# Kernel tuning notes

Measured on AMD Instinct MI355X. Metric: run time of the kernel, lower is better.

The kernel has to match this reference:

```python
import jax, jax.numpy as jnp
import numpy as np

Q_SCALE = 64  # 1 << 6, from quantize_8bit default
Q_STEP = 2.0 / Q_SCALE
Q_MIN = -(2 ** 7) / Q_SCALE      # -128/64 = -2.0
Q_MAX = (2 ** 7 - 1) / Q_SCALE   # 127/64


def quantize_8bit(x):
    # round-to-step with straight-through estimator (matches slayer quantize), then clamp
    xq = x + jax.lax.stop_gradient(jnp.round(x / Q_STEP) * Q_STEP - x)
    return jnp.clip(xq, Q_MIN, Q_MAX)


def weight_norm(v, g):
    # per-output-channel weight norm: w = g * v / ||v||  (v: [out, in])
    n = jnp.sqrt(jnp.sum(v * v, axis=1, keepdims=True))
    return g[:, None] * v / n


def sigma_delta_block(x, v, g, clamp6):
    # x: [N, Cin, H, W, T]
    qw = quantize_8bit(weight_norm(v, g))           # [Cout, Cin], 8-bit quantized
    y = jnp.einsum('oi,nihwt->nohwt', qw, x)        # 1x1x1 conv (pointwise)
    s = jnp.cumsum(y, axis=-1)                      # sigma unit: accumulate over time
    mean = jnp.mean(s, axis=(0, 2, 3, 4), keepdims=True)  # mean-only batchnorm
    a = s - mean
    if clamp6:                                      # Clamp6 activation (fc2); Ind = identity (fc1)
        a = jnp.clip(a, -6.0, 6.0)
    # delta unit, threshold=0: d[t] = a[t] - a[t-1], a[-1] = 0
    d = jnp.diff(a, axis=-1, prepend=jnp.zeros_like(a[..., :1]))
    return d


def setup_inputs() -> dict:
    key = jax.random.key(0)
    k = jax.random.split(key, 5)
    N, C, H, W, T = 4, 128, 32, 32, 32
    Cs = 32
    x = jax.random.normal(k[0], (N, C, H, W, T), dtype=jnp.float32)
    v1 = jax.random.normal(k[1], (Cs, C), dtype=jnp.float32) * 0.1
    g1 = jax.random.uniform(k[2], (Cs,), dtype=jnp.float32) + 0.5
    v2 = jax.random.normal(k[3], (C, Cs), dtype=jnp.float32) * 0.1
    g2 = jax.random.uniform(k[4], (C,), dtype=jnp.float32) + 0.5
    return {'x': x, 'v1': v1, 'g1': g1, 'v2': v2, 'g2': g2}


def reference(x, v1, g1, v2, g2):
    h = sigma_delta_block(x, v1, g1, clamp6=False)   # fc1: Ind activation
    out = sigma_delta_block(h, v2, g2, clamp6=True)  # fc2: Clamp6 activation
    return out
```

## Files before the change

kernel.cpp:

```cpp
#include <hip/hip_runtime.h>

#define CIN  128
#define CHUNKF 32768

typedef float f32x4 __attribute__((ext_vector_type(4)));
typedef short s16x8 __attribute__((ext_vector_type(8)));


__device__ __forceinline__ uint pack_hilo(float f) {
  uint b = __float_as_uint(f);
  uint hi = b & 0xffff0000u;
  float lo = f - __uint_as_float(hi);
  return (hi >> 16) | (__float_as_uint(lo) & 0xffff0000u);
}

__global__ __launch_bounds__(256) void wnorm_mean_kernel(
    const float* __restrict__ x,
    const float* __restrict__ v1, const float* __restrict__ g1,
    const float* __restrict__ v2, const float* __restrict__ g2,
    float* __restrict__ ws) {
  int tid = threadIdx.x;
  if (blockIdx.x < 2048) {
    int b = blockIdx.x;
    int chunk = b >> 2, quarter = b & 3;
    int i = chunk & 127;
    const float4* xp = (const float4*)(x + (size_t)chunk * CHUNKF + (size_t)quarter * 8192);
    float acc = 0.f;
#pragma unroll
    for (int it = 0; it < 8; ++it) {
      int f4i = tid + 256 * it;
      float4 v = xp[f4i];
      int t0 = (4 * f4i) & 31;
      acc += v.x * (float)(32 - t0) + v.y * (float)(31 - t0)
           + v.z * (float)(30 - t0) + v.w * (float)(29 - t0);
    }
    for (int off = 32; off >= 1; off >>= 1) acc += __shfl_down(acc, off);
    __shared__ float part[4];
    if ((tid & 63) == 0) part[tid >> 6] = acc;
    __syncthreads();
    if (tid == 0) atomicAdd(&ws[8192 + i], part[0] + part[1] + part[2] + part[3]);
  } else {
    int b = blockIdx.x - 2048;
    bool first = (b < 32);
    int row = first ? b : b - 32;
    int len = first ? 128 : 32;
    const float* v = first ? v1 : v2;
    const float* g = first ? g1 : g2;

    double val = 0.0;
    if (tid < len) { double t = (double)v[row * len + tid]; val = t * t; }
    for (int off = 32; off >= 1; off >>= 1) val += __shfl_down(val, off);
    __shared__ double partial[4];
    if ((tid & 63) == 0) partial[tid >> 6] = val;
    __syncthreads();
    double norm = sqrt(partial[0] + partial[1]);
    if (tid < len) {
      double w = (double)g[row] * (double)v[row * len + tid] / norm;
      double qd = rint(w * 32.0) * 0.03125;
      qd = fmin(fmax(qd, -2.0), 1.984375);
      float qf = (float)qd;
      ushort bf = (ushort)(__float_as_uint(qf) >> 16);
      if (first) {
        ws[row * 128 + tid] = qf;
        ((ushort*)(ws + 8448))[row * 128 + tid] = bf;
      } else {
        ws[4096 + row * 32 + tid] = qf;
        ((ushort*)(ws + 10496))[row * 32 + tid] = bf;
      }
    }
  }
}

__global__ __launch_bounds__(128) void kappa_kernel(float* __restrict__ ws) {
  __shared__ float z[32];
  int tid = threadIdx.x;
  const float* qw1 = ws;
  const float* qw2 = ws + 4096;
  const float* msum = ws + 8192;
  if (tid < 32) {
    float acc = 0.f;
    for (int c = 0; c < 128; ++c) acc += qw1[tid * 128 + c] * msum[c];
    z[tid] = acc * (1.0f / 131072.0f);
  }
  __syncthreads();
  float k = 0.f;
  for (int j = 0; j < 32; ++j) k += qw2[tid * 32 + j] * z[j];
  ws[8320 + tid] = k;
}

__global__ __launch_bounds__(256, 2) void fused_kernel(
    const float* __restrict__ x, const float* __restrict__ ws,
    float* __restrict__ out) {
  const ushort* qw1bf = (const ushort*)(ws + 8448);
  const ushort* qw2bf = (const ushort*)(ws + 10496);
  const float* kap = ws + 8320;

  __shared__ uint xs[8192];
  __shared__ uint zs[4096];

  const int tid = threadIdx.x;
  const int wv = tid >> 6;
  const int l  = tid & 63;
  const int g  = l >> 4;
  const int ln = l & 15;

  const int nb  = blockIdx.x >> 8;
  const int hw0 = (blockIdx.x & 255) * 4;
  const float* xblk = x + (size_t)nb * CIN * CHUNKF + (size_t)hw0 * 32;

  s16x8 A1[2][4];
#pragma unroll
  for (int jt = 0; jt < 2; ++jt)
#pragma unroll
    for (int ks = 0; ks < 4; ++ks)
      A1[jt][ks] = *(const s16x8*)(qw1bf + (jt * 16 + ln) * 128 + ks * 32 + g * 8);
  s16x8 B2[8];
  float kv[8];
#pragma unroll
  for (int nt = 0; nt < 8; ++nt) {
    B2[nt] = *(const s16x8*)(qw2bf + (nt * 16 + ln) * 32 + g * 8);
    kv[nt] = kap[nt * 16 + ln];
  }

  float4 xr[8];
#pragma unroll
  for (int k = 0; k < 8; ++k) {
    int f = k * 256 + tid, c = f >> 5, n4 = f & 31;
    xr[k] = *(const float4*)(xblk + (size_t)c * CHUNKF + n4 * 4);
  }

  f32x4 acc1[2][2];
#pragma unroll
  for (int a = 0; a < 2; ++a)
#pragma unroll
    for (int b = 0; b < 2; ++b) acc1[a][b] = (f32x4){0.f, 0.f, 0.f, 0.f};

#pragma unroll
  for (int ph = 0; ph < 2; ++ph) {
#pragma unroll
    for (int k = 0; k < 8; ++k) {
      int f = k * 256 + tid, c = f >> 5, n4 = f & 31;
      int u = n4 ^ ((c >> 2) & 6);
      uint4 pk;
      pk.x = pack_hilo(xr[k].x); pk.y = pack_hilo(xr[k].y);
      pk.z = pack_hilo(xr[k].z); pk.w = pack_hilo(xr[k].w);
      *(uint4*)&xs[c * 128 + u * 4] = pk;
    }
    __syncthreads();
    if (ph == 0) {
#pragma unroll
      for (int k = 0; k < 8; ++k) {
        int f = k * 256 + tid, c = f >> 5, n4 = f & 31;
        xr[k] = *(const float4*)(xblk + (size_t)(64 + c) * CHUNKF + n4 * 4);
      }
    }
#pragma unroll
    for (int kl = 0; kl < 2; ++kl) {
#pragma unroll
      for (int nt = 0; nt < 2; ++nt) {
        const int n = wv * 32 + nt * 16 + ln;
        uint q0, q1, q2, q3, q4, q5, q6, q7;
        {
          const int base = (kl * 32 + g * 8) * 128;
          const int u = ((n >> 2) ^ (((kl * 32 + g * 8) >> 2) & 6)) * 4 + (n & 3);
          q0 = xs[base + 0 * 128 + u]; q1 = xs[base + 1 * 128 + u];
          q2 = xs[base + 2 * 128 + u]; q3 = xs[base + 3 * 128 + u];
          q4 = xs[base + 4 * 128 + u]; q5 = xs[base + 5 * 128 + u];
          q6 = xs[base + 6 * 128 + u]; q7 = xs[base + 7 * 128 + u];
        }
        uint4 H, L;
        H.x = (q0 & 0xffffu) | (q1 << 16);  H.y = (q2 & 0xffffu) | (q3 << 16);
        H.z = (q4 & 0xffffu) | (q5 << 16);  H.w = (q6 & 0xffffu) | (q7 << 16);
        L.x = (q0 >> 16) | (q1 & 0xffff0000u); L.y = (q2 >> 16) | (q3 & 0xffff0000u);
        L.z = (q4 >> 16) | (q5 & 0xffff0000u); L.w = (q6 >> 16) | (q7 & 0xffff0000u);
        s16x8 Bh = __builtin_bit_cast(s16x8, H);
        s16x8 Bl = __builtin_bit_cast(s16x8, L);
#pragma unroll
        for (int jt = 0; jt < 2; ++jt) {
          acc1[jt][nt] = __builtin_amdgcn_mfma_f32_16x16x32_bf16(
              A1[jt][ph * 2 + kl], Bh, acc1[jt][nt], 0, 0, 0);
          acc1[jt][nt] = __builtin_amdgcn_mfma_f32_16x16x32_bf16(
              A1[jt][ph * 2 + kl], Bl, acc1[jt][nt], 0, 0, 0);
        }
      }
    }
    if (ph == 0) __syncthreads();
  }

  uint* zw = zs + wv * 1024;
#pragma unroll
  for (int jt = 0; jt < 2; ++jt)
#pragma unroll
    for (int nt = 0; nt < 2; ++nt) {
      int n = nt * 16 + ln;
      int u = (jt * 4 + g) ^ (n & 7);
      uint4 pk;
      pk.x = pack_hilo(acc1[jt][nt][0]);
      pk.y = pack_hilo(acc1[jt][nt][1]);
      pk.z = pack_hilo(acc1[jt][nt][2]);
      pk.w = pack_hilo(acc1[jt][nt][3]);
      *(uint4*)&zw[n * 32 + u * 4] = pk;
    }

  f32x4 acc2[8][2];
#pragma unroll
  for (int a = 0; a < 8; ++a)
#pragma unroll
    for (int b = 0; b < 2; ++b) acc2[a][b] = (f32x4){0.f, 0.f, 0.f, 0.f};

#pragma unroll
  for (int mt = 0; mt < 2; ++mt) {
    int n = mt * 16 + ln;
    int u0 = (2 * g) ^ (n & 7);
    int u1 = (2 * g + 1) ^ (n & 7);
    uint4 qa = *(const uint4*)&zw[n * 32 + u0 * 4];
    uint4 qb = *(const uint4*)&zw[n * 32 + u1 * 4];
    uint4 H, L;
    H.x = (qa.x & 0xffffu) | (qa.y << 16);  H.y = (qa.z & 0xffffu) | (qa.w << 16);
    H.z = (qb.x & 0xffffu) | (qb.y << 16);  H.w = (qb.z & 0xffffu) | (qb.w << 16);
    L.x = (qa.x >> 16) | (qa.y & 0xffff0000u); L.y = (qa.z >> 16) | (qa.w & 0xffff0000u);
    L.z = (qb.x >> 16) | (qb.y & 0xffff0000u); L.w = (qb.z >> 16) | (qb.w & 0xffff0000u);
    s16x8 Ah = __builtin_bit_cast(s16x8, H);
    s16x8 Al = __builtin_bit_cast(s16x8, L);
#pragma unroll
    for (int nt = 0; nt < 8; ++nt) {
      acc2[nt][mt] = __builtin_amdgcn_mfma_f32_16x16x32_bf16(Ah, B2[nt], acc2[nt][mt], 0, 0, 0);
      acc2[nt][mt] = __builtin_amdgcn_mfma_f32_16x16x32_bf16(Al, B2[nt], acc2[nt][mt], 0, 0, 0);
    }
  }

  const size_t outbase = (size_t)nb * CIN * CHUNKF + (size_t)(hw0 + wv) * 32;
#pragma unroll
  for (int nt = 0; nt < 8; ++nt) {
    float c0[2], c1[2], c2[2], c3[2], base[2], Qi0 = 0.f;
#pragma unroll
    for (int mt = 0; mt < 2; ++mt) {
      c0[mt] = acc2[nt][mt][0];
      c1[mt] = c0[mt] + acc2[nt][mt][1];
      c2[mt] = c1[mt] + acc2[nt][mt][2];
      c3[mt] = c2[mt] + acc2[nt][mt][3];
      float Qi = c3[mt];
      float t1 = __shfl_up(Qi, 16); if (g >= 1) Qi += t1;
      float t2 = __shfl_up(Qi, 32); if (g >= 2) Qi += t2;
      base[mt] = Qi - c3[mt];
      if (mt == 0) Qi0 = Qi;
    }
    float S0tot = __shfl(Qi0, 48 + ln);
    base[1] += S0tot;
    const float kpp = kv[nt];
    float* op = out + outbase + (size_t)(nt * 16 + ln) * CHUNKF;
#pragma unroll
    for (int mt = 0; mt < 2; ++mt) {
      float Bv = base[mt] - kpp;
      float prev = fminf(fmaxf(Bv, -6.f), 6.f);
      if (mt == 0 && g == 0) prev = 0.f;
      float A0 = fminf(fmaxf(Bv + c0[mt], -6.f), 6.f);
      float A1v = fminf(fmaxf(Bv + c1[mt], -6.f), 6.f);
      float A2v = fminf(fmaxf(Bv + c2[mt], -6.f), 6.f);
      float A3v = fminf(fmaxf(Bv + c3[mt], -6.f), 6.f);
      *(float4*)(op + mt * 16 + g * 4) =
          make_float4(A0 - prev, A1v - A0, A2v - A1v, A3v - A2v);
    }
  }
}

extern "C" void kernel_launch(void* const* d_in, const int* in_sizes, int n_in,
                              void* d_out, int out_size, void* d_ws, size_t ws_size,
                              hipStream_t stream) {
  const float* x  = (const float*)d_in[0];
  const float* v1 = (const float*)d_in[1];
  const float* g1 = (const float*)d_in[2];
  const float* v2 = (const float*)d_in[3];
  const float* g2 = (const float*)d_in[4];
  float* ws  = (float*)d_ws;
  float* out = (float*)d_out;

  hipMemsetAsync(ws + 8192, 0, 128 * sizeof(float), stream);
  wnorm_mean_kernel<<<2208, 256, 0, stream>>>(x, v1, g1, v2, g2, ws);
  kappa_kernel<<<1, 128, 0, stream>>>(ws);
  fused_kernel<<<1024, 256, 0, stream>>>(x, ws, out);
}
```

Baseline: 51.02 us.

## Fold kappa computation into fused kernel, reuse LDS, and raise occupancy

Removes the single-block kappa kernel launch and has every fused block recompute the mean-correction vector kappa from the workspace into shared memory. The z staging buffer now aliases the x LDS buffer, which needs an extra barrier after the second phase. The second GEMM is split into two halves with per-half B2 loads, cutting register pressure so launch bounds can request 4 blocks per CU. The trade is redundant per-block kappa arithmetic and extra syncs in exchange for one fewer launch and higher occupancy.

```diff
diff --git a/kernel.cpp b/kernel.cpp
--- a/kernel.cpp
+++ b/kernel.cpp
@@ -71,32 +71,15 @@
   }
 }
 
-__global__ __launch_bounds__(128) void kappa_kernel(float* __restrict__ ws) {
-  __shared__ float z[32];
-  int tid = threadIdx.x;
-  const float* qw1 = ws;
-  const float* qw2 = ws + 4096;
-  const float* msum = ws + 8192;
-  if (tid < 32) {
-    float acc = 0.f;
-    for (int c = 0; c < 128; ++c) acc += qw1[tid * 128 + c] * msum[c];
-    z[tid] = acc * (1.0f / 131072.0f);
-  }
-  __syncthreads();
-  float k = 0.f;
-  for (int j = 0; j < 32; ++j) k += qw2[tid * 32 + j] * z[j];
-  ws[8320 + tid] = k;
-}
-
-__global__ __launch_bounds__(256, 2) void fused_kernel(
+__global__ __launch_bounds__(256, 4) void fused_kernel(
     const float* __restrict__ x, const float* __restrict__ ws,
     float* __restrict__ out) {
   const ushort* qw1bf = (const ushort*)(ws + 8448);
   const ushort* qw2bf = (const ushort*)(ws + 10496);
-  const float* kap = ws + 8320;
 
   __shared__ uint xs[8192];
-  __shared__ uint zs[4096];
+  __shared__ float zred[288];
+  __shared__ float kls[128];
 
   const int tid = threadIdx.x;
   const int wv = tid >> 6;
@@ -108,25 +91,43 @@
   const int hw0 = (blockIdx.x & 255) * 4;
   const float* xblk = x + (size_t)nb * CIN * CHUNKF + (size_t)hw0 * 32;
 
-  s16x8 A1[2][4];
-#pragma unroll
-  for (int jt = 0; jt < 2; ++jt)
-#pragma unroll
-    for (int ks = 0; ks < 4; ++ks)
-      A1[jt][ks] = *(const s16x8*)(qw1bf + (jt * 16 + ln) * 128 + ks * 32 + g * 8);
-  s16x8 B2[8];
-  float kv[8];
-#pragma unroll
-  for (int nt = 0; nt < 8; ++nt) {
-    B2[nt] = *(const s16x8*)(qw2bf + (nt * 16 + ln) * 32 + g * 8);
-    kv[nt] = kap[nt * 16 + ln];
-  }
-
   float4 xr[8];
 #pragma unroll
   for (int k = 0; k < 8; ++k) {
     int f = k * 256 + tid, c = f >> 5, n4 = f & 31;
     xr[k] = *(const float4*)(xblk + (size_t)c * CHUNKF + n4 * 4);
+  }
+
+  s16x8 A1[2][4];
+#pragma unroll
+  for (int jt = 0; jt < 2; ++jt)
+#pragma unroll
+    for (int ks = 0; ks < 4; ++ks)
+      A1[jt][ks] = *(const s16x8*)(qw1bf + (jt * 16 + ln) * 128 + ks * 32 + g * 8);
+
+  {
+    int j = tid & 31, grp = tid >> 5;
+    const float* qr = ws + j * 128 + grp * 16;
+    const float* mr = ws + 8192 + grp * 16;
+    float pp = 0.f;
+#pragma unroll
+    for (int cc = 0; cc < 16; ++cc) pp += qr[cc] * mr[cc];
+    zred[j * 8 + grp] = pp;
+  }
+  __syncthreads();
+  if (tid < 32) {
+    float t = 0.f;
+#pragma unroll
+    for (int gg = 0; gg < 8; ++gg) t += zred[tid * 8 + gg];
+    zred[256 + tid] = t * (1.0f / 131072.0f);
+  }
+  __syncthreads();
+  if (tid < 128) {
+    const float* q2 = ws + 4096 + tid * 32;
+    float kk = 0.f;
+#pragma unroll 8
+    for (int j = 0; j < 32; ++j) kk += q2[j] * zred[256 + j];
+    kls[tid] = kk;
   }
 
   f32x4 acc1[2][2];
@@ -184,10 +185,10 @@
         }
       }
     }
-    if (ph == 0) __syncthreads();
-  }
-
-  uint* zw = zs + wv * 1024;
+    __syncthreads();
+  }
+
+  uint* zw = xs + wv * 1024;
 #pragma unroll
   for (int jt = 0; jt < 2; ++jt)
 #pragma unroll
@@ -202,12 +203,7 @@
       *(uint4*)&zw[n * 32 + u * 4] = pk;
     }
 
-  f32x4 acc2[8][2];
-#pragma unroll
-  for (int a = 0; a < 8; ++a)
-#pragma unroll
-    for (int b = 0; b < 2; ++b) acc2[a][b] = (f32x4){0.f, 0.f, 0.f, 0.f};
-
+  s16x8 Ah[2], Al[2];
 #pragma unroll
   for (int mt = 0; mt < 2; ++mt) {
     int n = mt * 16 + ln;
@@ -220,46 +216,64 @@
     H.z = (qb.x & 0xffffu) | (qb.y << 16);  H.w = (qb.z & 0xffffu) | (qb.w << 16);
     L.x = (qa.x >> 16) | (qa.y & 0xffff0000u); L.y = (qa.z >> 16) | (qa.w & 0xffff0000u);
     L.z = (qb.x >> 16) | (qb.y & 0xffff0000u); L.w = (qb.z >> 16) | (qb.w & 0xffff0000u);
-    s16x8 Ah = __builtin_bit_cast(s16x8, H);
-    s16x8 Al = __builtin_bit_cast(s16x8, L);
-#pragma unroll
-    for (int nt = 0; nt < 8; ++nt) {
-      acc2[nt][mt] = __builtin_amdgcn_mfma_f32_16x16x32_bf16(Ah, B2[nt], acc2[nt][mt], 0, 0, 0);
-      acc2[nt][mt] = __builtin_amdgcn_mfma_f32_16x16x32_bf16(Al, B2[nt], acc2[nt][mt], 0, 0, 0);
-    }
+    Ah[mt] = __builtin_bit_cast(s16x8, H);
+    Al[mt] = __builtin_bit_cast(s16x8, L);
   }
 
   const size_t outbase = (size_t)nb * CIN * CHUNKF + (size_t)(hw0 + wv) * 32;
-#pragma unroll
-  for (int nt = 0; nt < 8; ++nt) {
-    float c0[2], c1[2], c2[2], c3[2], base[2], Qi0 = 0.f;
-#pragma unroll
-    for (int mt = 0; mt < 2; ++mt) {
-      c0[mt] = acc2[nt][mt][0];
-      c1[mt] = c0[mt] + acc2[nt][mt][1];
-      c2[mt] = c1[mt] + acc2[nt][mt][2];
-      c3[mt] = c2[mt] + acc2[nt][mt][3];
-      float Qi = c3[mt];
-      float t1 = __shfl_up(Qi, 16); if (g >= 1) Qi += t1;
-      float t2 = __shfl_up(Qi, 32); if (g >= 2) Qi += t2;
-      base[mt] = Qi - c3[mt];
-      if (mt == 0) Qi0 = Qi;
-    }
-    float S0tot = __shfl(Qi0, 48 + ln);
-    base[1] += S0tot;
-    const float kpp = kv[nt];
-    float* op = out + outbase + (size_t)(nt * 16 + ln) * CHUNKF;
-#pragma unroll
-    for (int mt = 0; mt < 2; ++mt) {
-      float Bv = base[mt] - kpp;
-      float prev = fminf(fmaxf(Bv, -6.f), 6.f);
-      if (mt == 0 && g == 0) prev = 0.f;
-      float A0 = fminf(fmaxf(Bv + c0[mt], -6.f), 6.f);
-      float A1v = fminf(fmaxf(Bv + c1[mt], -6.f), 6.f);
-      float A2v = fminf(fmaxf(Bv + c2[mt], -6.f), 6.f);
-      float A3v = fminf(fmaxf(Bv + c3[mt], -6.f), 6.f);
-      *(float4*)(op + mt * 16 + g * 4) =
-          make_float4(A0 - prev, A1v - A0, A2v - A1v, A3v - A2v);
+#pragma unroll 1
+  for (int h = 0; h < 2; ++h) {
+    s16x8 B2[4];
+#pragma unroll
+    for (int q = 0; q < 4; ++q)
+      B2[q] = *(const s16x8*)(qw2bf + ((h * 4 + q) * 16 + ln) * 32 + g * 8);
+
+    f32x4 acc2[4][2];
+#pragma unroll
+    for (int a = 0; a < 4; ++a)
+#pragma unroll
+      for (int b = 0; b < 2; ++b) acc2[a][b] = (f32x4){0.f, 0.f, 0.f, 0.f};
+
+#pragma unroll
+    for (int mt = 0; mt < 2; ++mt)
+#pragma unroll
+      for (int q = 0; q < 4; ++q) {
+        acc2[q][mt] = __builtin_amdgcn_mfma_f32_16x16x32_bf16(Ah[mt], B2[q], acc2[q][mt], 0, 0, 0);
+        acc2[q][mt] = __builtin_amdgcn_mfma_f32_16x16x32_bf16(Al[mt], B2[q], acc2[q][mt], 0, 0, 0);
+      }
+
+#pragma unroll
+    for (int q = 0; q < 4; ++q) {
+      const int nt = h * 4 + q;
+      float c0[2], c1[2], c2[2], c3[2], base[2], Qi0 = 0.f;
+#pragma unroll
+      for (int mt = 0; mt < 2; ++mt) {
+        c0[mt] = acc2[q][mt][0];
+        c1[mt] = c0[mt] + acc2[q][mt][1];
+        c2[mt] = c1[mt] + acc2[q][mt][2];
+        c3[mt] = c2[mt] + acc2[q][mt][3];
+        float Qi = c3[mt];
+        float t1 = __shfl_up(Qi, 16); if (g >= 1) Qi += t1;
+        float t2 = __shfl_up(Qi, 32); if (g >= 2) Qi += t2;
+        base[mt] = Qi - c3[mt];
+        if (mt == 0) Qi0 = Qi;
+      }
+      float S0tot = __shfl(Qi0, 48 + ln);
+      base[1] += S0tot;
+      const float kpp = kls[nt * 16 + ln];
+      float* op = out + outbase + (size_t)(nt * 16 + ln) * CHUNKF;
+#pragma unroll
+      for (int mt = 0; mt < 2; ++mt) {
+        float Bv = base[mt] - kpp;
+        float prev = fminf(fmaxf(Bv, -6.f), 6.f);
+        if (mt == 0 && g == 0) prev = 0.f;
+        float A0 = fminf(fmaxf(Bv + c0[mt], -6.f), 6.f);
+        float A1v = fminf(fmaxf(Bv + c1[mt], -6.f), 6.f);
+        float A2v = fminf(fmaxf(Bv + c2[mt], -6.f), 6.f);
+        float A3v = fminf(fmaxf(Bv + c3[mt], -6.f), 6.f);
+        *(float4*)(op + mt * 16 + g * 4) =
+            make_float4(A0 - prev, A1v - A0, A2v - A1v, A3v - A2v);
+      }
     }
   }
 }
@@ -277,6 +291,5 @@
 
   hipMemsetAsync(ws + 8192, 0, 128 * sizeof(float), stream);
   wnorm_mean_kernel<<<2208, 256, 0, stream>>>(x, v1, g1, v2, g2, ws);
-  kappa_kernel<<<1, 128, 0, stream>>>(ws);
   fused_kernel<<<1024, 256, 0, stream>>>(x, ws, out);
 }
```

Measured after the change: 49.39 us. 3.2% less time.
